# Optimization experiments

Hardware: AMD Instinct MI355X
Metric: run time of the kernel (lower is better)

## Reference

```python
import jax, jax.numpy as jnp
import numpy as np

NUM_T = 1000
B, N = 16, 2048
M = 8192


def _cosine_alphas_cumprod(T=NUM_T, s=0.008):
    # Faithful to ColdDiffusion.cosine_beta_schedule + cumprod of (1 - betas)
    x = np.linspace(0.0, T, T + 1)
    ac = np.cos((x / T + s) / (1 + s) * np.pi * 0.5) ** 2
    ac = ac / ac[0]
    betas = np.clip(1.0 - ac[1:] / ac[:-1], 0.0001, 0.9999)
    return np.cumprod(1.0 - betas)


def setup_inputs() -> dict:
    key = jax.random.key(0)
    k1, k2, k3 = jax.random.split(key, 3)
    x_start = jax.random.normal(k1, (B, N, 4, 2), dtype=jnp.float32)
    anchors = jax.random.normal(k2, (M, 4, 2), dtype=jnp.float32)
    t = jax.random.randint(k3, (B,), 0, NUM_T)
    ac = _cosine_alphas_cumprod()
    sqrt_alphas_cumprod = jnp.asarray(np.sqrt(ac), dtype=jnp.float32)
    sqrt_one_minus_alphas_cumprod = jnp.asarray(np.sqrt(1.0 - ac), dtype=jnp.float32)
    return {
        "x_start": x_start,
        "anchors": anchors,
        "sqrt_alphas_cumprod": sqrt_alphas_cumprod,
        "sqrt_one_minus_alphas_cumprod": sqrt_one_minus_alphas_cumprod,
        "t": t,
    }


def reference(x_start, anchors, sqrt_alphas_cumprod, sqrt_one_minus_alphas_cumprod, t):
    # q_sample with anchor matching, fully batched (no Python loop over B).
    Bq, Nq = x_start.shape[:2]
    xf = x_start.reshape(Bq, Nq, -1)            # [B,N,8]
    af = anchors.reshape(anchors.shape[0], -1)  # [M,8]
    scores = jnp.einsum('bnd,md->bnm', xf, af) * (-2.0) + jnp.sum(af * af, axis=-1)  # [B,N,M]
    idx = jnp.argmin(scores, axis=-1)           # [B,N]
    matched = anchors[idx]                      # [B,N,4,2] gather
    sa = sqrt_alphas_cumprod[t][:, None, None, None]                 # [B,1,1,1]
    sb = sqrt_one_minus_alphas_cumprod[t][:, None, None, None]       # [B,1,1,1]
    return sa * x_start + sb * matched
```

## Files before the change

kernel.cpp:

```cpp
#include <hip/hip_runtime.h>
#include <stdint.h>

#define B_      16
#define N_      2048
#define M_      8192
#define ROWS    (B_ * N_)
#define D_      8

#define SPLITS  32
#define MSPLIT  (M_ / SPLITS)
#define BLK     256
#define RPT     8
#define ROWS_PER_BLK (BLK * RPT)
#define ROWBLKS (ROWS / ROWS_PER_BLK)

#define TPR     8
#define BROWS   32


__global__ __launch_bounds__(BLK, 2) void argmin_part_kernel(
    const float* __restrict__ x,
    const float* __restrict__ anchors,
    float* __restrict__ ws)
{
    __shared__ float sA[MSPLIT * D_];
    __shared__ float sH[MSPLIT];

    const int split = blockIdx.y;
    const int tid   = threadIdx.x;

    const float4* gA = (const float4*)(anchors + (size_t)split * MSPLIT * D_);
    #pragma unroll
    for (int i = 0; i < 2; ++i) {
        const int k = tid + i * BLK;
        const float4 g = gA[k];
        ((float4*)sA)[k] = (float4){-g.x, -g.y, -g.z, -g.w};
    }
    __syncthreads();

    {
        const float* na = &sA[tid * D_];
        float nr = na[0] * na[0];
        #pragma unroll
        for (int k = 1; k < D_; ++k) nr = fmaf(na[k], na[k], nr);
        sH[tid] = 0.5f * nr;
    }
    __syncthreads();

    const int row0 = blockIdx.x * ROWS_PER_BLK + tid;
    float X[RPT][D_];
    #pragma unroll
    for (int r = 0; r < RPT; ++r) {
        const float4* px = (const float4*)(x + (size_t)(row0 + r * BLK) * D_);
        const float4 lo = px[0], hi = px[1];
        X[r][0] = lo.x; X[r][1] = lo.y; X[r][2] = lo.z; X[r][3] = lo.w;
        X[r][4] = hi.x; X[r][5] = hi.y; X[r][6] = hi.z; X[r][7] = hi.w;
    }

    float best[RPT];
    #pragma unroll
    for (int r = 0; r < RPT; ++r) best[r] = 3.4e38f;

    #pragma unroll 2
    for (int j = 0; j < MSPLIT; ++j) {
        const float4 a0 = ((const float4*)sA)[j * 2];
        const float4 a1 = ((const float4*)sA)[j * 2 + 1];
        const float  hn = sH[j];
        #pragma unroll
        for (int r = 0; r < RPT; ++r) {
            float s = fmaf(X[r][0], a0.x, hn);
            s = fmaf(X[r][1], a0.y, s);
            s = fmaf(X[r][2], a0.z, s);
            s = fmaf(X[r][3], a0.w, s);
            s = fmaf(X[r][4], a1.x, s);
            s = fmaf(X[r][5], a1.y, s);
            s = fmaf(X[r][6], a1.z, s);
            s = fmaf(X[r][7], a1.w, s);
            best[r] = fminf(best[r], s);
        }
    }

    #pragma unroll
    for (int r = 0; r < RPT; ++r)
        ws[(size_t)split * ROWS + (row0 + r * BLK)] = best[r];
}

__global__ __launch_bounds__(256) void refine_combine_kernel(
    const float* __restrict__ x,
    const float* __restrict__ anchors,
    const float* __restrict__ sa_tab,
    const float* __restrict__ sb_tab,
    const int*   __restrict__ t,
    const float* __restrict__ ws,
    float* __restrict__ out)
{
    const int tid  = threadIdx.x;
    const int g    = tid & (TPR - 1);
    const int rloc = tid >> 3;
    const int row  = blockIdx.x * BROWS + rloc;

    float bs = 3.4e38f;
    int bsplit = 0;
    #pragma unroll
    for (int k = 0; k < SPLITS / TPR; ++k) {
        const int s = g + k * TPR;
        const float v = ws[(size_t)s * ROWS + row];
        const bool c = v < bs;
        bs     = c ? v : bs;
        bsplit = c ? s : bsplit;
    }
    #pragma unroll
    for (int m = 1; m < TPR; m <<= 1) {
        const float ov  = __shfl_xor(bs, m);
        const int   osp = __shfl_xor(bsplit, m);
        const bool take = (ov < bs) || (ov == bs && osp < bsplit);
        bs     = take ? ov  : bs;
        bsplit = take ? osp : bsplit;
    }
    const uint32_t target = __float_as_uint(bs);
    const int base = bsplit * MSPLIT;

    const float4* px = (const float4*)(x + (size_t)row * D_);
    const float4 xlo = px[0], xhi = px[1];
    const float X0 = xlo.x, X1 = xlo.y, X2 = xlo.z, X3 = xlo.w;
    const float X4 = xhi.x, X5 = xhi.y, X6 = xhi.z, X7 = xhi.w;

    int mloc = 0x7FFFFFFF;
    #pragma unroll 4
    for (int j = 0; j < MSPLIT / TPR; ++j) {
        const int ai = base + j * TPR + g;
        const float4* pa = (const float4*)(anchors + (size_t)ai * D_);
        const float4 g0 = pa[0], g1 = pa[1];
        const float na0 = -g0.x, na1 = -g0.y, na2 = -g0.z, na3 = -g0.w;
        const float na4 = -g1.x, na5 = -g1.y, na6 = -g1.z, na7 = -g1.w;
        float nr = na0 * na0;
        nr = fmaf(na1, na1, nr);
        nr = fmaf(na2, na2, nr);
        nr = fmaf(na3, na3, nr);
        nr = fmaf(na4, na4, nr);
        nr = fmaf(na5, na5, nr);
        nr = fmaf(na6, na6, nr);
        nr = fmaf(na7, na7, nr);
        const float hn = 0.5f * nr;
        float s = fmaf(X0, na0, hn);
        s = fmaf(X1, na1, s);
        s = fmaf(X2, na2, s);
        s = fmaf(X3, na3, s);
        s = fmaf(X4, na4, s);
        s = fmaf(X5, na5, s);
        s = fmaf(X6, na6, s);
        s = fmaf(X7, na7, s);
        const bool m = (__float_as_uint(s) == target);
        mloc = (m && ai < mloc) ? ai : mloc;
    }
    #pragma unroll
    for (int m = 1; m < TPR; m <<= 1) {
        const int o = __shfl_xor(mloc, m);
        mloc = (o < mloc) ? o : mloc;
    }
    const int bi = (mloc == 0x7FFFFFFF) ? base : mloc;

    if (g == 0) {
        const int b  = row >> 11;
        const int tb = t[b];
        const float sa = sa_tab[tb];
        const float sb = sb_tab[tb];

        const float4* pa = (const float4*)(anchors + (size_t)bi * D_);
        const float4 a0 = pa[0], a1 = pa[1];

        float4 o0, o1;
        o0.x = fmaf(sa, xlo.x, sb * a0.x);
        o0.y = fmaf(sa, xlo.y, sb * a0.y);
        o0.z = fmaf(sa, xlo.z, sb * a0.z);
        o0.w = fmaf(sa, xlo.w, sb * a0.w);
        o1.x = fmaf(sa, xhi.x, sb * a1.x);
        o1.y = fmaf(sa, xhi.y, sb * a1.y);
        o1.z = fmaf(sa, xhi.z, sb * a1.z);
        o1.w = fmaf(sa, xhi.w, sb * a1.w);

        float4* po = (float4*)(out + (size_t)row * D_);
        po[0] = o0;
        po[1] = o1;
    }
}

extern "C" void kernel_launch(void* const* d_in, const int* in_sizes, int n_in,
                              void* d_out, int out_size, void* d_ws, size_t ws_size,
                              hipStream_t stream) {
    const float* x       = (const float*)d_in[0];
    const float* anchors = (const float*)d_in[1];
    const float* sa_tab  = (const float*)d_in[2];
    const float* sb_tab  = (const float*)d_in[3];
    const int*   t       = (const int*)d_in[4];
    float* out = (float*)d_out;

    float* ws = (float*)d_ws;

    dim3 gridA(ROWBLKS, SPLITS);
    argmin_part_kernel<<<gridA, BLK, 0, stream>>>(x, anchors, ws);

    refine_combine_kernel<<<ROWS / BROWS, 256, 0, stream>>>(
        x, anchors, sa_tab, sb_tab, t, ws, out);
}
```

Before: 125.4 us.

## Read anchors via uniform global loads instead of LDS and halve rows per thread

```diff
diff --git a/kernel.cpp b/kernel.cpp
--- a/kernel.cpp
+++ b/kernel.cpp
@@ -10,7 +10,7 @@
 #define SPLITS  32
 #define MSPLIT  (M_ / SPLITS)
 #define BLK     256
-#define RPT     8
+#define RPT     4
 #define ROWS_PER_BLK (BLK * RPT)
 #define ROWBLKS (ROWS / ROWS_PER_BLK)
 
@@ -18,31 +18,31 @@
 #define BROWS   32
 
 
-__global__ __launch_bounds__(BLK, 2) void argmin_part_kernel(
+__global__ __launch_bounds__(BLK)
+__attribute__((amdgpu_waves_per_eu(4, 4)))
+void argmin_part_kernel(
     const float* __restrict__ x,
     const float* __restrict__ anchors,
     float* __restrict__ ws)
 {
-    __shared__ float sA[MSPLIT * D_];
     __shared__ float sH[MSPLIT];
 
     const int split = blockIdx.y;
     const int tid   = threadIdx.x;
 
-    const float4* gA = (const float4*)(anchors + (size_t)split * MSPLIT * D_);
-    #pragma unroll
-    for (int i = 0; i < 2; ++i) {
-        const int k = tid + i * BLK;
-        const float4 g = gA[k];
-        ((float4*)sA)[k] = (float4){-g.x, -g.y, -g.z, -g.w};
-    }
-    __syncthreads();
-
     {
-        const float* na = &sA[tid * D_];
-        float nr = na[0] * na[0];
-        #pragma unroll
-        for (int k = 1; k < D_; ++k) nr = fmaf(na[k], na[k], nr);
+        const float4* pa = (const float4*)(anchors + (size_t)(split * MSPLIT + tid) * D_);
+        const float4 g0 = pa[0], g1 = pa[1];
+        const float na0 = -g0.x, na1 = -g0.y, na2 = -g0.z, na3 = -g0.w;
+        const float na4 = -g1.x, na5 = -g1.y, na6 = -g1.z, na7 = -g1.w;
+        float nr = na0 * na0;
+        nr = fmaf(na1, na1, nr);
+        nr = fmaf(na2, na2, nr);
+        nr = fmaf(na3, na3, nr);
+        nr = fmaf(na4, na4, nr);
+        nr = fmaf(na5, na5, nr);
+        nr = fmaf(na6, na6, nr);
+        nr = fmaf(na7, na7, nr);
         sH[tid] = 0.5f * nr;
     }
     __syncthreads();
@@ -61,21 +61,23 @@
     #pragma unroll
     for (int r = 0; r < RPT; ++r) best[r] = 3.4e38f;
 
-    #pragma unroll 2
+    const float4* gA = (const float4*)(anchors + (size_t)split * MSPLIT * D_);
+
+    #pragma unroll 4
     for (int j = 0; j < MSPLIT; ++j) {
-        const float4 a0 = ((const float4*)sA)[j * 2];
-        const float4 a1 = ((const float4*)sA)[j * 2 + 1];
+        const float4 a0 = gA[2 * j];
+        const float4 a1 = gA[2 * j + 1];
         const float  hn = sH[j];
         #pragma unroll
         for (int r = 0; r < RPT; ++r) {
-            float s = fmaf(X[r][0], a0.x, hn);
-            s = fmaf(X[r][1], a0.y, s);
-            s = fmaf(X[r][2], a0.z, s);
-            s = fmaf(X[r][3], a0.w, s);
-            s = fmaf(X[r][4], a1.x, s);
-            s = fmaf(X[r][5], a1.y, s);
-            s = fmaf(X[r][6], a1.z, s);
-            s = fmaf(X[r][7], a1.w, s);
+            float s = fmaf(X[r][0], -a0.x, hn);
+            s = fmaf(X[r][1], -a0.y, s);
+            s = fmaf(X[r][2], -a0.z, s);
+            s = fmaf(X[r][3], -a0.w, s);
+            s = fmaf(X[r][4], -a1.x, s);
+            s = fmaf(X[r][5], -a1.y, s);
+            s = fmaf(X[r][6], -a1.z, s);
+            s = fmaf(X[r][7], -a1.w, s);
             best[r] = fminf(best[r], s);
         }
     }
```

New measurement: 138.7 us. 10.6% more time.

## Compute anchor scores with split-bf16 MFMA and track argmin indices directly

Applied to the files above, without the earlier changes.

```diff
diff --git a/kernel.cpp b/kernel.cpp
--- a/kernel.cpp
+++ b/kernel.cpp
@@ -7,182 +7,220 @@
 #define ROWS    (B_ * N_)
 #define D_      8
 
-#define SPLITS  32
-#define MSPLIT  (M_ / SPLITS)
-#define BLK     256
-#define RPT     8
-#define ROWS_PER_BLK (BLK * RPT)
-#define ROWBLKS (ROWS / ROWS_PER_BLK)
-
-#define TPR     8
-#define BROWS   32
-
-
-__global__ __launch_bounds__(BLK, 2) void argmin_part_kernel(
+#define QUARTERS 4
+#define APQ     (M_ / QUARTERS)
+#define CHUNK   256
+#define NCHUNK  (APQ / CHUNK)
+#define TPC     (CHUNK / 16)
+#define WROWS   64
+#define BROWS_A 256
+#define GRIDX   (ROWS / BROWS_A)
+
+#define OFF_NH  0
+#define OFF_NM  4096
+#define OFF_NL  8192
+#define OFF_HN  12288
+#define BUFSTRIDE 16384
+#define SMEM_BYTES 49152
+
+
+typedef short bf16x8 __attribute__((ext_vector_type(8)));
+typedef float f32x4  __attribute__((ext_vector_type(4)));
+
+__device__ __forceinline__ unsigned short f2bf(float f) {
+    unsigned u = __float_as_uint(f);
+    u += 0x7FFFu + ((u >> 16) & 1u);
+    return (unsigned short)(u >> 16);
+}
+__device__ __forceinline__ float bf2f(unsigned short h) {
+    return __uint_as_float(((unsigned)h) << 16);
+}
+
+__device__ __forceinline__ void stage_store(char* buf, int i, float4 g0, float4 g1) {
+    float nv[8] = {-g0.x, -g0.y, -g0.z, -g0.w, -g1.x, -g1.y, -g1.z, -g1.w};
+    bf16x8 vh, vm, vl;
+    #pragma unroll
+    for (int k = 0; k < 8; ++k) {
+        unsigned short h = f2bf(nv[k]);
+        float r1 = nv[k] - bf2f(h);
+        unsigned short m = f2bf(r1);
+        float r2 = r1 - bf2f(m);
+        unsigned short l = f2bf(r2);
+        vh[k] = (short)h; vm[k] = (short)m; vl[k] = (short)l;
+    }
+    *(bf16x8*)(buf + OFF_NH + i * 16) = vh;
+    *(bf16x8*)(buf + OFF_NM + i * 16) = vm;
+    *(bf16x8*)(buf + OFF_NL + i * 16) = vl;
+    float nr = nv[0] * nv[0];
+    #pragma unroll
+    for (int k = 1; k < 8; ++k) nr = fmaf(nv[k], nv[k], nr);
+    *(float*)(buf + OFF_HN + i * 4) = 0.5f * nr;
+}
+
+__global__ __launch_bounds__(256) void argmin_mfma_kernel(
     const float* __restrict__ x,
     const float* __restrict__ anchors,
-    float* __restrict__ ws)
+    float* __restrict__ wsv,
+    int*   __restrict__ wsi)
 {
-    __shared__ float sA[MSPLIT * D_];
-    __shared__ float sH[MSPLIT];
-
-    const int split = blockIdx.y;
-    const int tid   = threadIdx.x;
-
-    const float4* gA = (const float4*)(anchors + (size_t)split * MSPLIT * D_);
-    #pragma unroll
-    for (int i = 0; i < 2; ++i) {
-        const int k = tid + i * BLK;
-        const float4 g = gA[k];
-        ((float4*)sA)[k] = (float4){-g.x, -g.y, -g.z, -g.w};
+    __shared__ __align__(16) char smem[SMEM_BYTES];
+
+    const int tid  = threadIdx.x;
+    const int wave = tid >> 6;
+    const int lane = tid & 63;
+    const int n    = lane & 15;
+    const int kb   = lane >> 4;
+
+    const int quarter = blockIdx.y;
+    const int abase   = quarter * APQ;
+    const int wrow0   = blockIdx.x * BROWS_A + wave * WROWS;
+
+    bf16x8 A1[4], A2[4];
+    #pragma unroll
+    for (int rt = 0; rt < 4; ++rt) {
+        const int row = wrow0 + rt * 16 + n;
+        const float4* px = (const float4*)(x + (size_t)row * D_);
+        const float4 lo = px[0], hi = px[1];
+        const float v[8] = {lo.x, lo.y, lo.z, lo.w, hi.x, hi.y, hi.z, hi.w};
+        const bool odd = (kb & 1);
+        const bool is2 = (kb == 2);
+        #pragma unroll
+        for (int k = 0; k < 8; ++k) {
+            unsigned short xh = f2bf(v[k]);
+            float r1 = v[k] - bf2f(xh);
+            unsigned short xm = f2bf(r1);
+            float r2 = r1 - bf2f(xm);
+            unsigned short xl = f2bf(r2);
+            A1[rt][k] = (short)(odd ? xm : xh);
+            A2[rt][k] = (short)(odd ? xl : (is2 ? xm : xh));
+        }
+    }
+
+    const int o1 = ((kb < 2) ? OFF_NH : OFF_NM) + n * 16;
+    const int o2 = ((kb == 1) ? OFF_NH : (kb == 3) ? OFF_NM : OFF_NL) + n * 16;
+    const int oh = OFF_HN + n * 4;
+
+    float best[4][4];
+    int   bidx[4][4];
+    #pragma unroll
+    for (int rt = 0; rt < 4; ++rt) {
+        #pragma unroll
+        for (int q = 0; q < 4; ++q) { best[rt][q] = 3.4e38f; bidx[rt][q] = 0; }
+    }
+
+    int idxv = abase + n;
+
+    {
+        const float4* pa = (const float4*)(anchors + (size_t)(abase + tid) * D_);
+        stage_store(smem, tid, pa[0], pa[1]);
     }
     __syncthreads();
 
-    {
-        const float* na = &sA[tid * D_];
-        float nr = na[0] * na[0];
-        #pragma unroll
-        for (int k = 1; k < D_; ++k) nr = fmaf(na[k], na[k], nr);
-        sH[tid] = 0.5f * nr;
-    }
-    __syncthreads();
-
-    const int row0 = blockIdx.x * ROWS_PER_BLK + tid;
-    float X[RPT][D_];
-    #pragma unroll
-    for (int r = 0; r < RPT; ++r) {
-        const float4* px = (const float4*)(x + (size_t)(row0 + r * BLK) * D_);
-        const float4 lo = px[0], hi = px[1];
-        X[r][0] = lo.x; X[r][1] = lo.y; X[r][2] = lo.z; X[r][3] = lo.w;
-        X[r][4] = hi.x; X[r][5] = hi.y; X[r][6] = hi.z; X[r][7] = hi.w;
-    }
-
-    float best[RPT];
-    #pragma unroll
-    for (int r = 0; r < RPT; ++r) best[r] = 3.4e38f;
-
-    #pragma unroll 2
-    for (int j = 0; j < MSPLIT; ++j) {
-        const float4 a0 = ((const float4*)sA)[j * 2];
-        const float4 a1 = ((const float4*)sA)[j * 2 + 1];
-        const float  hn = sH[j];
-        #pragma unroll
-        for (int r = 0; r < RPT; ++r) {
-            float s = fmaf(X[r][0], a0.x, hn);
-            s = fmaf(X[r][1], a0.y, s);
-            s = fmaf(X[r][2], a0.z, s);
-            s = fmaf(X[r][3], a0.w, s);
-            s = fmaf(X[r][4], a1.x, s);
-            s = fmaf(X[r][5], a1.y, s);
-            s = fmaf(X[r][6], a1.z, s);
-            s = fmaf(X[r][7], a1.w, s);
-            best[r] = fminf(best[r], s);
-        }
-    }
-
-    #pragma unroll
-    for (int r = 0; r < RPT; ++r)
-        ws[(size_t)split * ROWS + (row0 + r * BLK)] = best[r];
-}
-
-__global__ __launch_bounds__(256) void refine_combine_kernel(
+    #pragma unroll 1
+    for (int c = 0; c < NCHUNK; ++c) {
+        const int bsel = c & 1;
+        char* bufr = smem + bsel * BUFSTRIDE;
+
+        float4 g0, g1;
+        if (c < NCHUNK - 1) {
+            const float4* pa = (const float4*)(
+                anchors + (size_t)(abase + (c + 1) * CHUNK + tid) * D_);
+            g0 = pa[0]; g1 = pa[1];
+        }
+
+        #pragma unroll
+        for (int tt = 0; tt < TPC; ++tt) {
+            const bf16x8 b1 = *(const bf16x8*)(bufr + o1 + tt * 256);
+            const bf16x8 b2 = *(const bf16x8*)(bufr + o2 + tt * 256);
+            const float  hn = *(const float*)(bufr + oh + tt * 64);
+            const f32x4 cvec = {hn, hn, hn, hn};
+            #pragma unroll
+            for (int rt = 0; rt < 4; ++rt) {
+                f32x4 acc = __builtin_amdgcn_mfma_f32_16x16x32_bf16(A1[rt], b1, cvec, 0, 0, 0);
+                acc = __builtin_amdgcn_mfma_f32_16x16x32_bf16(A2[rt], b2, acc, 0, 0, 0);
+                #pragma unroll
+                for (int q = 0; q < 4; ++q) {
+                    const bool lt = acc[q] < best[rt][q];
+                    best[rt][q] = lt ? acc[q] : best[rt][q];
+                    bidx[rt][q] = lt ? idxv   : bidx[rt][q];
+                }
+            }
+            idxv += 16;
+        }
+
+        if (c < NCHUNK - 1)
+            stage_store(smem + (bsel ^ 1) * BUFSTRIDE, tid, g0, g1);
+        __syncthreads();
+    }
+
+    #pragma unroll
+    for (int rt = 0; rt < 4; ++rt) {
+        #pragma unroll
+        for (int q = 0; q < 4; ++q) {
+            float bv = best[rt][q]; int bi = bidx[rt][q];
+            #pragma unroll
+            for (int m = 1; m < 16; m <<= 1) {
+                const float ov = __shfl_xor(bv, m);
+                const int   oi = __shfl_xor(bi, m);
+                const bool take = (ov < bv) || (ov == bv && oi < bi);
+                bv = take ? ov : bv;
+                bi = take ? oi : bi;
+            }
+            if ((lane & 15) == 0) {
+                const int row = wrow0 + rt * 16 + (lane >> 4) * 4 + q;
+                wsv[(size_t)quarter * ROWS + row] = bv;
+                wsi[(size_t)quarter * ROWS + row] = bi;
+            }
+        }
+    }
+}
+
+__global__ __launch_bounds__(256) void combine_kernel(
     const float* __restrict__ x,
     const float* __restrict__ anchors,
     const float* __restrict__ sa_tab,
     const float* __restrict__ sb_tab,
     const int*   __restrict__ t,
-    const float* __restrict__ ws,
+    const float* __restrict__ wsv,
+    const int*   __restrict__ wsi,
     float* __restrict__ out)
 {
-    const int tid  = threadIdx.x;
-    const int g    = tid & (TPR - 1);
-    const int rloc = tid >> 3;
-    const int row  = blockIdx.x * BROWS + rloc;
-
-    float bs = 3.4e38f;
-    int bsplit = 0;
-    #pragma unroll
-    for (int k = 0; k < SPLITS / TPR; ++k) {
-        const int s = g + k * TPR;
-        const float v = ws[(size_t)s * ROWS + row];
-        const bool c = v < bs;
-        bs     = c ? v : bs;
-        bsplit = c ? s : bsplit;
-    }
-    #pragma unroll
-    for (int m = 1; m < TPR; m <<= 1) {
-        const float ov  = __shfl_xor(bs, m);
-        const int   osp = __shfl_xor(bsplit, m);
-        const bool take = (ov < bs) || (ov == bs && osp < bsplit);
-        bs     = take ? ov  : bs;
-        bsplit = take ? osp : bsplit;
-    }
-    const uint32_t target = __float_as_uint(bs);
-    const int base = bsplit * MSPLIT;
+    const int row = blockIdx.x * 256 + threadIdx.x;
+
+    float bv = wsv[row];
+    int   bi = wsi[row];
+    #pragma unroll
+    for (int qq = 1; qq < QUARTERS; ++qq) {
+        const float v = wsv[(size_t)qq * ROWS + row];
+        const int   i = wsi[(size_t)qq * ROWS + row];
+        const bool take = (v < bv) || (v == bv && i < bi);
+        bv = take ? v : bv;
+        bi = take ? i : bi;
+    }
+
+    const int b  = row >> 11;
+    const int tb = t[b];
+    const float sa = sa_tab[tb];
+    const float sb = sb_tab[tb];
 
     const float4* px = (const float4*)(x + (size_t)row * D_);
     const float4 xlo = px[0], xhi = px[1];
-    const float X0 = xlo.x, X1 = xlo.y, X2 = xlo.z, X3 = xlo.w;
-    const float X4 = xhi.x, X5 = xhi.y, X6 = xhi.z, X7 = xhi.w;
-
-    int mloc = 0x7FFFFFFF;
-    #pragma unroll 4
-    for (int j = 0; j < MSPLIT / TPR; ++j) {
-        const int ai = base + j * TPR + g;
-        const float4* pa = (const float4*)(anchors + (size_t)ai * D_);
-        const float4 g0 = pa[0], g1 = pa[1];
-        const float na0 = -g0.x, na1 = -g0.y, na2 = -g0.z, na3 = -g0.w;
-        const float na4 = -g1.x, na5 = -g1.y, na6 = -g1.z, na7 = -g1.w;
-        float nr = na0 * na0;
-        nr = fmaf(na1, na1, nr);
-        nr = fmaf(na2, na2, nr);
-        nr = fmaf(na3, na3, nr);
-        nr = fmaf(na4, na4, nr);
-        nr = fmaf(na5, na5, nr);
-        nr = fmaf(na6, na6, nr);
-        nr = fmaf(na7, na7, nr);
-        const float hn = 0.5f * nr;
-        float s = fmaf(X0, na0, hn);
-        s = fmaf(X1, na1, s);
-        s = fmaf(X2, na2, s);
-        s = fmaf(X3, na3, s);
-        s = fmaf(X4, na4, s);
-        s = fmaf(X5, na5, s);
-        s = fmaf(X6, na6, s);
-        s = fmaf(X7, na7, s);
-        const bool m = (__float_as_uint(s) == target);
-        mloc = (m && ai < mloc) ? ai : mloc;
-    }
-    #pragma unroll
-    for (int m = 1; m < TPR; m <<= 1) {
-        const int o = __shfl_xor(mloc, m);
-        mloc = (o < mloc) ? o : mloc;
-    }
-    const int bi = (mloc == 0x7FFFFFFF) ? base : mloc;
-
-    if (g == 0) {
-        const int b  = row >> 11;
-        const int tb = t[b];
-        const float sa = sa_tab[tb];
-        const float sb = sb_tab[tb];
-
-        const float4* pa = (const float4*)(anchors + (size_t)bi * D_);
-        const float4 a0 = pa[0], a1 = pa[1];
-
-        float4 o0, o1;
-        o0.x = fmaf(sa, xlo.x, sb * a0.x);
-        o0.y = fmaf(sa, xlo.y, sb * a0.y);
-        o0.z = fmaf(sa, xlo.z, sb * a0.z);
-        o0.w = fmaf(sa, xlo.w, sb * a0.w);
-        o1.x = fmaf(sa, xhi.x, sb * a1.x);
-        o1.y = fmaf(sa, xhi.y, sb * a1.y);
-        o1.z = fmaf(sa, xhi.z, sb * a1.z);
-        o1.w = fmaf(sa, xhi.w, sb * a1.w);
-
-        float4* po = (float4*)(out + (size_t)row * D_);
-        po[0] = o0;
-        po[1] = o1;
-    }
+    const float4* pa = (const float4*)(anchors + (size_t)bi * D_);
+    const float4 a0 = pa[0], a1 = pa[1];
+
+    float4 o0, o1;
+    o0.x = fmaf(sa, xlo.x, sb * a0.x);
+    o0.y = fmaf(sa, xlo.y, sb * a0.y);
+    o0.z = fmaf(sa, xlo.z, sb * a0.z);
+    o0.w = fmaf(sa, xlo.w, sb * a0.w);
+    o1.x = fmaf(sa, xhi.x, sb * a1.x);
+    o1.y = fmaf(sa, xhi.y, sb * a1.y);
+    o1.z = fmaf(sa, xhi.z, sb * a1.z);
+    o1.w = fmaf(sa, xhi.w, sb * a1.w);
+
+    float4* po = (float4*)(out + (size_t)row * D_);
+    po[0] = o0;
+    po[1] = o1;
 }
 
 extern "C" void kernel_launch(void* const* d_in, const int* in_sizes, int n_in,
@@ -195,11 +233,12 @@
     const int*   t       = (const int*)d_in[4];
     float* out = (float*)d_out;
 
-    float* ws = (float*)d_ws;
-
-    dim3 gridA(ROWBLKS, SPLITS);
-    argmin_part_kernel<<<gridA, BLK, 0, stream>>>(x, anchors, ws);
-
-    refine_combine_kernel<<<ROWS / BROWS, 256, 0, stream>>>(
-        x, anchors, sa_tab, sb_tab, t, ws, out);
-}
+    float* wsv = (float*)d_ws;
+    int*   wsi = (int*)((char*)d_ws + (size_t)QUARTERS * ROWS * sizeof(float));
+
+    dim3 gridA(GRIDX, QUARTERS);
+    argmin_mfma_kernel<<<gridA, 256, 0, stream>>>(x, anchors, wsv, wsi);
+
+    combine_kernel<<<ROWS / 256, 256, 0, stream>>>(
+        x, anchors, sa_tab, sb_tab, t, wsv, wsi, out);
+}
```

Result: slower. 167.3 us (+33.4%).
